# Performance work log

Measured on AMD Instinct MI355X. Metric: run time of the kernel, lower is better.

The kernel has to match this reference:

```python
import jax, jax.numpy as jnp
import numpy as np
import math

LOG_2PI = math.log(2.0 * math.pi)


def setup_inputs() -> dict:
    key = jax.random.key(0)
    k_x, k_mu = jax.random.split(key, 2)
    B, T, S, M, D = 8, 4096, 64, 8, 128
    return {
        "X": jax.random.normal(k_x, (B, T, D), dtype=jnp.float32),
        "pi_logits": jnp.zeros((S,), dtype=jnp.float32),
        "trans_logits": jnp.zeros((S, S), dtype=jnp.float32),
        "weight_logits": jnp.zeros((S, M), dtype=jnp.float32),
        "means": jax.random.normal(k_mu, (S, M, D), dtype=jnp.float32),
        "log_vars": jnp.zeros((S, M, D), dtype=jnp.float32),
    }


def reference(X, pi_logits, trans_logits, weight_logits, means, log_vars):
    # X: [B,T,D]; means/log_vars: [S,M,D]
    D = X.shape[-1]
    inv_vars = jnp.exp(-log_vars)                                   # [S,M,D]
    # -0.5 * sum_d (x_d - mu_d)^2 / var_d, expanded as GEMMs (same math):
    a = jnp.einsum('btd,smd->btsm', X * X, inv_vars)                # sum x^2/var
    b = jnp.einsum('btd,smd->btsm', X, means * inv_vars)            # sum x*mu/var
    c = jnp.sum(means * means * inv_vars, axis=-1)                  # [S,M]
    exp_term = -0.5 * (a - 2.0 * b + c[None, None, :, :])           # [B,T,S,M]
    log_norm = -0.5 * (jnp.sum(log_vars, axis=-1) + D * LOG_2PI)    # [S,M]
    log_mix_w = jax.nn.log_softmax(weight_logits, axis=1)           # [S,M]
    # emission log-prob per state: logsumexp over mixture components
    emis = jax.scipy.special.logsumexp(
        exp_term + (log_norm + log_mix_w)[None, None], axis=-1)     # [B,T,S]

    log_pi = jax.nn.log_softmax(pi_logits)                          # [S]
    log_A = jax.nn.log_softmax(trans_logits, axis=1)                # [S,S]

    alpha0 = log_pi[None, :] + emis[:, 0]                           # [B,S]
    emis_t = jnp.swapaxes(emis, 0, 1)                               # [T,B,S]

    def step(alpha, e_t):
        # alpha: [B,S]; log-semiring matvec: logsumexp_i(alpha_i + A_ij)
        nxt = e_t + jax.scipy.special.logsumexp(
            alpha[:, :, None] + log_A[None, :, :], axis=1)
        return nxt, None

    alpha_T, _ = jax.lax.scan(step, alpha0, emis_t[1:])
    return jax.scipy.special.logsumexp(alpha_T, axis=-1)            # [B]
```

## Files before the change

kernel.cpp:

```cpp
#include <hip/hip_runtime.h>
#include <hip/hip_bf16.h>
#include <math.h>

#define LOG2PI_F 1.8378770664093453f

typedef __attribute__((ext_vector_type(8))) short bf16x8;
typedef __attribute__((ext_vector_type(4))) float f32x4;
typedef __attribute__((ext_vector_type(16))) float f32x16;

static __device__ inline short f2bf(float x) {
  __hip_bfloat16 h = __float2bfloat16(x);
  return *reinterpret_cast<short*>(&h);
}
static __device__ inline unsigned cvtpk(float lo, float hi) {
  unsigned r;
  asm("v_cvt_pk_bf16_f32 %0, %1, %2" : "=v"(r) : "v"(lo), "v"(hi));
  return r;
}
static __device__ inline f32x4 mfma16(bf16x8 a, bf16x8 b, f32x4 c) {
  return __builtin_amdgcn_mfma_f32_16x16x32_bf16(a, b, c, 0, 0, 0);
}
static __device__ inline f32x16 mfma32(bf16x8 a, bf16x8 b, f32x16 c) {
  return __builtin_amdgcn_mfma_f32_32x32x16_bf16(a, b, c, 0, 0, 0);
}

__global__ __launch_bounds__(256) void mmm_prep_fused(
    const float* __restrict__ tl, const float* __restrict__ means,
    const float* __restrict__ log_vars, const float* __restrict__ weight_logits,
    const float* __restrict__ X,
    short* __restrict__ WTbf, short* __restrict__ Gt,
    float* __restrict__ const_c, short* __restrict__ XeP) {
  __shared__ float red[4];
  int bid = blockIdx.x;
  int tid = threadIdx.x;

  if (bid < 64) {
    if (tid < 64) {
      int r = bid, lane = tid;
      float v = tl[r * 64 + lane];
      float mx = v;
      #pragma unroll
      for (int off = 1; off < 64; off <<= 1) mx = fmaxf(mx, __shfl_xor(mx, off));
      float e = expf(v - mx);
      float s = e;
      #pragma unroll
      for (int off = 1; off < 64; off <<= 1) s += __shfl_xor(s, off);
      WTbf[lane * 64 + r] = f2bf(e / s);
    }
    return;
  }

  if (bid < 320) {
    int h = tid >> 7, d = tid & 127;
    int sm = (bid - 64) * 2 + h;
    int s = sm >> 3, m = sm & 7;
    float lv = log_vars[sm * 128 + d];
    float iv = expf(-lv);
    float mu = means[sm * 128 + d];
    float miv = mu * iv;
    Gt[sm * 256 + d] = f2bf(miv);
    Gt[sm * 256 + 128 + d] = f2bf(-0.5f * iv);
    float v = mu * miv + lv;
    #pragma unroll
    for (int off = 1; off < 64; off <<= 1) v += __shfl_xor(v, off);
    if ((tid & 63) == 0) red[tid >> 6] = v;
    __syncthreads();
    if (d == 0) {
      float tot = red[2 * h] + red[2 * h + 1];
      float wl[8];
      float mx = -3.4e38f;
      #pragma unroll
      for (int j = 0; j < 8; ++j) { wl[j] = weight_logits[s * 8 + j]; mx = fmaxf(mx, wl[j]); }
      float sum = 0.f;
      #pragma unroll
      for (int j = 0; j < 8; ++j) sum += expf(wl[j] - mx);
      float lmw = wl[m] - mx - logf(sum);
      const_c[sm] = -0.5f * (tot + 128.0f * LOG2PI_F) + lmw;
    }
    return;
  }

  int kbid = bid - 320;
  int q = kbid >> 7;
  int bt = ((kbid & 127) << 8) + tid;
  const float4* src = (const float4*)(X + (size_t)bt * 128 + q * 32);
  float xv[32];
  #pragma unroll
  for (int i = 0; i < 8; ++i) {
    float4 v = src[i];
    xv[4 * i] = v.x; xv[4 * i + 1] = v.y; xv[4 * i + 2] = v.z; xv[4 * i + 3] = v.w;
  }
  size_t base1 = ((size_t)q * 32768 + bt) * 32;
  size_t base2 = ((size_t)(q + 4) * 32768 + bt) * 32;
  int bx = bt & 3;
  #pragma unroll
  for (int g = 0; g < 4; ++g) {
    unsigned w1[4], w2[4];
    #pragma unroll
    for (int j = 0; j < 4; ++j) {
      float a = xv[g * 8 + 2 * j], c = xv[g * 8 + 2 * j + 1];
      w1[j] = cvtpk(a, c);
      w2[j] = cvtpk(a * a, c * c);
    }
    int gs = (g ^ bx) * 8;
    *(uint4*)&XeP[base1 + gs] = *(uint4*)w1;
    *(uint4*)&XeP[base2 + gs] = *(uint4*)w2;
  }
}

__global__ __launch_bounds__(512) void mmm_emis_kernel(
    const short* __restrict__ Gt, const short* __restrict__ XeP,
    const float* __restrict__ const_c,
    float* __restrict__ ehat, float* __restrict__ cmax) {
  __shared__ __align__(16) short Bt[16384];
  __shared__ __align__(16) float ccs[512];
  __shared__ float wavemax[8][64];
  __shared__ float colmax[64];
  int tid = threadIdx.x;
  int w = tid >> 6, lane = tid & 63, lr = lane & 15, lg = lane >> 4;

  ccs[tid] = const_c[tid];

  bf16x8 gf[4][8];
  #pragma unroll
  for (int rt = 0; rt < 4; ++rt) {
    int row = w * 64 + rt * 16 + lr;
    #pragma unroll
    for (int kc = 0; kc < 8; ++kc)
      gf[rt][kc] = *(const bf16x8*)&Gt[row * 256 + kc * 32 + lg * 8];
  }

  uint4 sreg[4];
  {
    size_t bt0 = (size_t)blockIdx.x * 64;
    #pragma unroll
    for (int r = 0; r < 4; ++r) {
      int ofs = r * 8192 + tid * 16;
      int kb2 = ofs >> 12, rem = ofs & 4095;
      sreg[r] = *(const uint4*)((const char*)XeP + ((size_t)kb2 * 32768 + bt0) * 64 + rem);
    }
  }

  for (int it = 0; it < 2; ++it) {
    int bt0 = (blockIdx.x + it * 256) * 64;
    __syncthreads();
    #pragma unroll
    for (int r = 0; r < 4; ++r)
      *(uint4*)((char*)Bt + r * 8192 + tid * 16) = sreg[r];
    __syncthreads();
    if (it == 0) {
      size_t bt0n = ((size_t)blockIdx.x + 256) * 64;
      #pragma unroll
      for (int r = 0; r < 4; ++r) {
        int ofs = r * 8192 + tid * 16;
        int kb2 = ofs >> 12, rem = ofs & 4095;
        sreg[r] = *(const uint4*)((const char*)XeP + ((size_t)kb2 * 32768 + bt0n) * 64 + rem);
      }
    }

    f32x4 acc[4][4];
    #pragma unroll
    for (int rt = 0; rt < 4; ++rt)
      #pragma unroll
      for (int ct = 0; ct < 4; ++ct)
        acc[rt][ct] = (f32x4){0.f, 0.f, 0.f, 0.f};

    #pragma unroll
    for (int kc = 0; kc < 8; ++kc) {
      bf16x8 bfr[4];
      #pragma unroll
      for (int ct = 0; ct < 4; ++ct) {
        int btL = ct * 16 + lr;
        bfr[ct] = *(const bf16x8*)&Bt[kc * 2048 + btL * 32 + ((lg ^ (btL & 3)) * 8)];
      }
      #pragma unroll
      for (int rt = 0; rt < 4; ++rt)
        #pragma unroll
        for (int ct = 0; ct < 4; ++ct)
          acc[rt][ct] = mfma16(gf[rt][kc], bfr[ct], acc[rt][ct]);
    }

    float lse[4][4];
    #pragma unroll
    for (int rt = 0; rt < 4; ++rt) {
      f32x4 cc = *(f32x4*)&ccs[w * 64 + rt * 16 + lg * 4];
      #pragma unroll
      for (int ct = 0; ct < 4; ++ct) {
        f32x4 v = acc[rt][ct] + cc;
        float mx = fmaxf(fmaxf(v[0], v[1]), fmaxf(v[2], v[3]));
        mx = fmaxf(mx, __shfl_xor(mx, 16));
        float sum = expf(v[0] - mx) + expf(v[1] - mx) + expf(v[2] - mx) + expf(v[3] - mx);
        sum += __shfl_xor(sum, 16);
        lse[rt][ct] = mx + logf(sum);
      }
    }
    #pragma unroll
    for (int ct = 0; ct < 4; ++ct) {
      float cm = fmaxf(fmaxf(lse[0][ct], lse[1][ct]), fmaxf(lse[2][ct], lse[3][ct]));
      cm = fmaxf(cm, __shfl_xor(cm, 32));
      if (lg == 0) wavemax[w][ct * 16 + lr] = cm;
    }
    __syncthreads();
    if (w == 0) {
      float cm = wavemax[0][lane];
      #pragma unroll
      for (int ww = 1; ww < 8; ++ww) cm = fmaxf(cm, wavemax[ww][lane]);
      colmax[lane] = cm;
      cmax[(size_t)bt0 + lane] = cm;
    }
    __syncthreads();
    #pragma unroll
    for (int ct = 0; ct < 4; ++ct) {
      float cm = colmax[ct * 16 + lr];
      #pragma unroll
      for (int rt = 0; rt < 4; ++rt) {
        float v = expf(lse[rt][ct] - cm);
        if (!(lg & 1))
          ehat[((size_t)bt0 + ct * 16 + lr) * 64 + (w * 8 + rt * 2 + (lg >> 1))] = v;
      }
    }
  }
}

__global__ __launch_bounds__(64) void mmm_chunk_kernel(
    const short* __restrict__ WTbf, const float* __restrict__ ehat,
    const float* __restrict__ cmax, short* __restrict__ NTb,
    float* __restrict__ aux) {
  __shared__ __align__(16) float elds[1024];
  int chunk = blockIdx.x, b = blockIdx.y;
  int lane = threadIdx.x;
  int l31 = lane & 31, hi = lane >> 5;

  int t0 = (chunk == 0) ? 1 : chunk * 16;
  int nsteps = (chunk == 0) ? 15 : 16;
  const float* eb = ehat + (size_t)b * 4096 * 64;

  {
    const float* esrc = eb + (size_t)t0 * 64;
    #pragma unroll
    for (int r = 0; r < 4; ++r)
      *(f32x4*)&elds[r * 256 + lane * 4] = *(const f32x4*)&esrc[r * 256 + lane * 4];
  }

  bf16x8 af[2][4];
  #pragma unroll
  for (int wi = 0; wi < 2; ++wi)
    #pragma unroll
    for (int kb = 0; kb < 4; ++kb)
      af[wi][kb] = *(const bf16x8*)&WTbf[(wi * 32 + l31) * 64 + kb * 16 + hi * 8];

  unsigned P[2][2][4][2];
  #pragma unroll
  for (int s = 0; s < 2; ++s) {
    int col = s * 32 + l31;
    #pragma unroll
    for (int cm = 0; cm < 2; ++cm)
      #pragma unroll
      for (int q = 0; q < 4; ++q)
        #pragma unroll
        for (int p = 0; p < 2; ++p) {
          int row = 32 * cm + 8 * q + 4 * hi + 2 * p;
          unsigned lo = (row == col) ? 0x3F80u : 0u;
          unsigned h16 = (row + 1 == col) ? 0x3F80u : 0u;
          P[s][cm][q][p] = lo | (h16 << 16);
        }
  }

  __syncthreads();

  float logscale = 0.f;
  f32x4 ecur[2][4], enxt[2][4];
  #pragma unroll
  for (int cm = 0; cm < 2; ++cm)
    #pragma unroll
    for (int q = 0; q < 4; ++q)
      ecur[cm][q] = *(const f32x4*)&elds[cm * 32 + q * 8 + hi * 4];

  for (int it = 0; it < nsteps; ++it) {
    if (it + 1 < nsteps) {
      #pragma unroll
      for (int cm = 0; cm < 2; ++cm)
        #pragma unroll
        for (int q = 0; q < 4; ++q)
          enxt[cm][q] = *(const f32x4*)&elds[(it + 1) * 64 + cm * 32 + q * 8 + hi * 4];
    }

    __builtin_amdgcn_s_setprio(1);
    #pragma unroll
    for (int s = 0; s < 2; ++s) {
      bf16x8 B[4];
      #pragma unroll
      for (int kb = 0; kb < 4; ++kb) {
        int cm = kb >> 1, kbl = kb & 1;
        int4 wrd;
        #pragma unroll
        for (int p = 0; p < 2; ++p) {
          unsigned avv = P[s][cm][2 * kbl + 1][p];
          unsigned bvv = P[s][cm][2 * kbl][p];
          asm("v_permlane32_swap_b32 %0, %1" : "+v"(avv), "+v"(bvv));
          if (p == 0) { wrd.x = (int)bvv; wrd.z = (int)avv; }
          else        { wrd.y = (int)bvv; wrd.w = (int)avv; }
        }
        B[kb] = *(bf16x8*)&wrd;
      }

      f32x16 d0, d1;
      #pragma unroll
      for (int r = 0; r < 16; ++r) { d0[r] = 0.f; d1[r] = 0.f; }
      #pragma unroll
      for (int kb = 0; kb < 4; ++kb) {
        d0 = mfma32(af[0][kb], B[kb], d0);
        d1 = mfma32(af[1][kb], B[kb], d1);
      }

      #pragma unroll
      for (int q = 0; q < 4; ++q)
        #pragma unroll
        for (int p = 0; p < 2; ++p) {
          P[s][0][q][p] = cvtpk(d0[4 * q + 2 * p] * ecur[0][q][2 * p],
                                d0[4 * q + 2 * p + 1] * ecur[0][q][2 * p + 1]);
          P[s][1][q][p] = cvtpk(d1[4 * q + 2 * p] * ecur[1][q][2 * p],
                                d1[4 * q + 2 * p + 1] * ecur[1][q][2 * p + 1]);
        }
    }
    __builtin_amdgcn_s_setprio(0);

    if ((it & 7) == 7) {
      float m = 0.f;
      #pragma unroll
      for (int s = 0; s < 2; ++s)
        #pragma unroll
        for (int cm = 0; cm < 2; ++cm)
          #pragma unroll
          for (int q = 0; q < 4; ++q)
            #pragma unroll
            for (int p = 0; p < 2; ++p) {
              unsigned u = P[s][cm][q][p];
              m = fmaxf(m, __uint_as_float(u << 16));
              m = fmaxf(m, __uint_as_float(u & 0xffff0000u));
            }
      #pragma unroll
      for (int off = 1; off < 64; off <<= 1) m = fmaxf(m, __shfl_xor(m, off));
      float inv = 1.0f / m;
      #pragma unroll
      for (int s = 0; s < 2; ++s)
        #pragma unroll
        for (int cm = 0; cm < 2; ++cm)
          #pragma unroll
          for (int q = 0; q < 4; ++q)
            #pragma unroll
            for (int p = 0; p < 2; ++p) {
              unsigned u = P[s][cm][q][p];
              P[s][cm][q][p] = cvtpk(__uint_as_float(u << 16) * inv,
                                     __uint_as_float(u & 0xffff0000u) * inv);
            }
      logscale += logf(m);
    }

    #pragma unroll
    for (int cm = 0; cm < 2; ++cm)
      #pragma unroll
      for (int q = 0; q < 4; ++q) ecur[cm][q] = enxt[cm][q];
  }

  unsigned short* No = (unsigned short*)(NTb + (((size_t)b * 256 + chunk) << 12));
  #pragma unroll
  for (int s = 0; s < 2; ++s)
    #pragma unroll
    for (int cm = 0; cm < 2; ++cm)
      #pragma unroll
      for (int q = 0; q < 4; ++q)
        #pragma unroll
        for (int p = 0; p < 2; ++p) {
          int row = 32 * cm + 8 * q + 4 * hi + 2 * p;
          int col = s * 32 + l31;
          unsigned u = P[s][cm][q][p];
          No[row * 64 + col] = (unsigned short)(u & 0xffffu);
          No[(row + 1) * 64 + col] = (unsigned short)(u >> 16);
        }

  float cs = (lane < nsteps) ? cmax[(size_t)b * 4096 + t0 + lane] : 0.f;
  #pragma unroll
  for (int off = 1; off < 64; off <<= 1) cs += __shfl_xor(cs, off);
  if (lane == 0) aux[(size_t)b * 256 + chunk] = cs + logscale;
}

__global__ __launch_bounds__(256) void mmm_merge_kernel(
    const short* __restrict__ NTb, const float* __restrict__ aux,
    float* __restrict__ G2T, float* __restrict__ auxg) {
  int g = blockIdx.x, b = blockIdx.y;
  int tid = threadIdx.x;
  int w = tid >> 6, lane = tid & 63;
  int wi = w >> 1, wj = w & 1;
  int lr = lane & 15, lg = lane >> 4;

  __shared__ __align__(16) short L[2][4096];
  __shared__ float wmax[4];

  for (int idx = tid; idx < 4096; idx += 256) {
    int j = idx >> 6, k = idx & 63;
    L[0][idx ^ ((j & 7) << 3)] = (j == k) ? (short)0x3F80 : (short)0;
  }
  __syncthreads();

  int cbase = b * 256 + g * 8;

  float logscale = 0.f;
  int cur = 0;
  f32x4 acc[2][2];

  bf16x8 apre[2][2];
  {
    const short* Mc = NTb + ((size_t)cbase << 12);
    #pragma unroll
    for (int rt = 0; rt < 2; ++rt)
      #pragma unroll
      for (int kc = 0; kc < 2; ++kc)
        apre[rt][kc] = *(const bf16x8*)&Mc[(wi * 32 + rt * 16 + lr) * 64 + kc * 32 + lg * 8];
  }

  for (int cc = 0; cc < 8; ++cc) {
    bf16x8 acur[2][2];
    #pragma unroll
    for (int rt = 0; rt < 2; ++rt)
      #pragma unroll
      for (int kc = 0; kc < 2; ++kc) acur[rt][kc] = apre[rt][kc];
    if (cc < 7) {
      const short* Mc = NTb + ((size_t)(cbase + cc + 1) << 12);
      #pragma unroll
      for (int rt = 0; rt < 2; ++rt)
        #pragma unroll
        for (int kc = 0; kc < 2; ++kc)
          apre[rt][kc] = *(const bf16x8*)&Mc[(wi * 32 + rt * 16 + lr) * 64 + kc * 32 + lg * 8];
    }

    logscale += aux[cbase + cc];

    bf16x8 bfr[2][2];
    #pragma unroll
    for (int ct = 0; ct < 2; ++ct) {
      int j = wj * 32 + ct * 16 + lr;
      int sw = (j & 7) << 3;
      #pragma unroll
      for (int kc = 0; kc < 2; ++kc)
        bfr[ct][kc] = *(const bf16x8*)&L[cur][(j * 64 + kc * 32 + lg * 8) ^ sw];
    }

    #pragma unroll
    for (int rt = 0; rt < 2; ++rt)
      #pragma unroll
      for (int ct = 0; ct < 2; ++ct) {
        f32x4 c = {0.f, 0.f, 0.f, 0.f};
        c = mfma16(acur[rt][0], bfr[ct][0], c);
        c = mfma16(acur[rt][1], bfr[ct][1], c);
        acc[rt][ct] = c;
      }

    if ((cc & 3) == 3) {
      float m = 0.f;
      #pragma unroll
      for (int rt = 0; rt < 2; ++rt)
        #pragma unroll
        for (int ct = 0; ct < 2; ++ct)
          #pragma unroll
          for (int r = 0; r < 4; ++r) m = fmaxf(m, acc[rt][ct][r]);
      #pragma unroll
      for (int off = 1; off < 64; off <<= 1) m = fmaxf(m, __shfl_xor(m, off));
      if (lane == 0) wmax[w] = m;
      __syncthreads();
      m = fmaxf(fmaxf(wmax[0], wmax[1]), fmaxf(wmax[2], wmax[3]));
      float inv = 1.0f / m;
      #pragma unroll
      for (int rt = 0; rt < 2; ++rt)
        #pragma unroll
        for (int ct = 0; ct < 2; ++ct) acc[rt][ct] *= inv;
      logscale += logf(m);
    }

    int nxt = cur ^ 1;
    unsigned* L32 = (unsigned*)&L[nxt][0];
    #pragma unroll
    for (int rt = 0; rt < 2; ++rt)
      #pragma unroll
      for (int ct = 0; ct < 2; ++ct) {
        int row0 = wi * 32 + rt * 16 + lg * 4;
        int col = wj * 32 + ct * 16 + lr;
        int sidx = (col * 64 + row0) ^ ((col & 7) << 3);
        L32[(sidx >> 1) + 0] = cvtpk(acc[rt][ct][0], acc[rt][ct][1]);
        L32[(sidx >> 1) + 1] = cvtpk(acc[rt][ct][2], acc[rt][ct][3]);
      }
    __syncthreads();
    cur = nxt;
  }

  float* Mo = G2T + (((size_t)b * 32 + g) << 12);
  #pragma unroll
  for (int rt = 0; rt < 2; ++rt)
    #pragma unroll
    for (int ct = 0; ct < 2; ++ct)
      #pragma unroll
      for (int r = 0; r < 4; ++r) {
        int row = wi * 32 + rt * 16 + lg * 4 + r;
        int col = wj * 32 + ct * 16 + lr;
        Mo[row * 64 + col] = acc[rt][ct][r];
      }

  if (w == 0 && lane == 0) auxg[b * 32 + g] = logscale;
}

__global__ __launch_bounds__(64) void mmm_combine_kernel(
    const float* __restrict__ pi_logits, const float* __restrict__ ehat,
    const float* __restrict__ cmax, const float* __restrict__ G2T,
    const float* __restrict__ auxg, float* __restrict__ out) {
  int b = blockIdx.x, lane = threadIdx.x;
  __shared__ __align__(16) float alds[64];

  float pv = pi_logits[lane];
  float mx = pv;
  #pragma unroll
  for (int off = 1; off < 64; off <<= 1) mx = fmaxf(mx, __shfl_xor(mx, off));
  float pe = expf(pv - mx);
  float ps = pe;
  #pragma unroll
  for (int off = 1; off < 64; off <<= 1) ps += __shfl_xor(ps, off);

  float a = (pe / ps) * ehat[(size_t)b * 4096 * 64 + lane];
  double logtot = (double)cmax[(size_t)b * 4096];
  alds[lane] = a;
  __builtin_amdgcn_wave_barrier();

  const float* Mb = G2T + (((size_t)b * 32) << 12) + lane * 64;
  f32x4 mc[16], mn[16];
  #pragma unroll
  for (int i = 0; i < 16; ++i) mc[i] = *(const f32x4*)&Mb[i * 4];

  for (int g = 0; g < 32; ++g) {
    if (g < 31) {
      const float* Mn = Mb + ((size_t)(g + 1) << 12);
      #pragma unroll
      for (int i = 0; i < 16; ++i) mn[i] = *(const f32x4*)&Mn[i * 4];
    }
    f32x4 a4 = {0.f, 0.f, 0.f, 0.f};
    #pragma unroll
    for (int i = 0; i < 16; ++i) {
      f32x4 av = *(const f32x4*)&alds[i * 4];
      a4 += mc[i] * av;
    }
    float acc = (a4[0] + a4[1]) + (a4[2] + a4[3]);
    float s = acc;
    #pragma unroll
    for (int off = 1; off < 64; off <<= 1) s += __shfl_xor(s, off);
    logtot += (double)(auxg[b * 32 + g] + logf(s));
    float an = acc / s;
    __builtin_amdgcn_wave_barrier();
    alds[lane] = an;
    __builtin_amdgcn_wave_barrier();
    #pragma unroll
    for (int i = 0; i < 16; ++i) mc[i] = mn[i];
  }
  if (lane == 0) out[b] = (float)logtot;
}

extern "C" void kernel_launch(void* const* d_in, const int* in_sizes, int n_in,
                              void* d_out, int out_size, void* d_ws, size_t ws_size,
                              hipStream_t stream) {
  const float* X      = (const float*)d_in[0];
  const float* pi_l   = (const float*)d_in[1];
  const float* tr_l   = (const float*)d_in[2];
  const float* wl     = (const float*)d_in[3];
  const float* means  = (const float*)d_in[4];
  const float* lvs    = (const float*)d_in[5];
  float* out = (float*)d_out;

  float* ws = (float*)d_ws;
  short* Gt      = (short*)ws;
  float* const_c = ws + 65536;
  short* WTbf    = (short*)(ws + 66048);
  float* cmaxp   = ws + 68608;
  float* ehat    = ws + 101376;
  short* XeP     = (short*)(ws + 2198528);
  short* NTb     = (short*)(ws + 2198528);
  float* aux     = ws + 6392832;
  float* G2T     = ws + 6396928;
  float* auxg    = ws + 7445504;

  mmm_prep_fused<<<832, 256, 0, stream>>>(tr_l, means, lvs, wl, X,
                                          WTbf, Gt, const_c, XeP);
  mmm_emis_kernel<<<256, 512, 0, stream>>>(Gt, XeP, const_c, ehat, cmaxp);
  mmm_chunk_kernel<<<dim3(256, 8), 64, 0, stream>>>(WTbf, ehat, cmaxp, NTb, aux);
  mmm_merge_kernel<<<dim3(32, 8), 256, 0, stream>>>(NTb, aux, G2T, auxg);
  mmm_combine_kernel<<<8, 64, 0, stream>>>(pi_l, ehat, cmaxp, G2T, auxg, out);
}
```

Baseline: 113.7 us.

## Fuse emission and chunk-product kernels through shared memory

Merges the emission kernel and the per-chunk transition-product kernel into one launch. Scaled emissions and column maxima now stay in LDS and feed the 16-step chunk recurrences directly, with 8 waves each handling one chunk. The full ehat/cmax round trip through global memory and one launch are removed, and only the t=0 values are kept for the combine step. In exchange the chunk work now runs on 256 blocks of 512 threads instead of 2048 single-wave blocks, which lowers parallelism, and LDS use per block grows by 32KB, which may cut occupancy.

```diff
diff --git a/kernel.cpp b/kernel.cpp
--- a/kernel.cpp
+++ b/kernel.cpp
@@ -108,16 +108,19 @@
   }
 }
 
-__global__ __launch_bounds__(512) void mmm_emis_kernel(
+__global__ __launch_bounds__(512) void mmm_emischunk_kernel(
     const short* __restrict__ Gt, const short* __restrict__ XeP,
-    const float* __restrict__ const_c,
-    float* __restrict__ ehat, float* __restrict__ cmax) {
+    const float* __restrict__ const_c, const short* __restrict__ WTbf,
+    short* __restrict__ NTb, float* __restrict__ aux,
+    float* __restrict__ ehat0, float* __restrict__ cmax0) {
   __shared__ __align__(16) short Bt[16384];
   __shared__ __align__(16) float ccs[512];
   __shared__ float wavemax[8][64];
-  __shared__ float colmax[64];
+  __shared__ float colmax2[2][64];
+  __shared__ __align__(16) float elds[2][4096];
   int tid = threadIdx.x;
   int w = tid >> 6, lane = tid & 63, lr = lane & 15, lg = lane >> 4;
+  int T0 = (blockIdx.x & 63) * 64;
 
   ccs[tid] = const_c[tid];
 
@@ -142,7 +145,7 @@
   }
 
   for (int it = 0; it < 2; ++it) {
-    int bt0 = (blockIdx.x + it * 256) * 64;
+    int bcur = (blockIdx.x + it * 256) >> 6;
     __syncthreads();
     #pragma unroll
     for (int r = 0; r < 4; ++r)
@@ -205,42 +208,33 @@
       float cm = wavemax[0][lane];
       #pragma unroll
       for (int ww = 1; ww < 8; ++ww) cm = fmaxf(cm, wavemax[ww][lane]);
-      colmax[lane] = cm;
-      cmax[(size_t)bt0 + lane] = cm;
+      colmax2[it][lane] = cm;
+      if (lane == 0 && T0 == 0) cmax0[bcur] = cm;
     }
     __syncthreads();
     #pragma unroll
     for (int ct = 0; ct < 4; ++ct) {
-      float cm = colmax[ct * 16 + lr];
+      float cm = colmax2[it][ct * 16 + lr];
       #pragma unroll
       for (int rt = 0; rt < 4; ++rt) {
         float v = expf(lse[rt][ct] - cm);
-        if (!(lg & 1))
-          ehat[((size_t)bt0 + ct * 16 + lr) * 64 + (w * 8 + rt * 2 + (lg >> 1))] = v;
-      }
-    }
-  }
-}
-
-__global__ __launch_bounds__(64) void mmm_chunk_kernel(
-    const short* __restrict__ WTbf, const float* __restrict__ ehat,
-    const float* __restrict__ cmax, short* __restrict__ NTb,
-    float* __restrict__ aux) {
-  __shared__ __align__(16) float elds[1024];
-  int chunk = blockIdx.x, b = blockIdx.y;
-  int lane = threadIdx.x;
+        if (!(lg & 1)) {
+          int s = w * 8 + rt * 2 + (lg >> 1);
+          elds[it][(ct * 16 + lr) * 64 + s] = v;
+          if (T0 == 0 && ct == 0 && lr == 0) ehat0[bcur * 64 + s] = v;
+        }
+      }
+    }
+  }
+  __syncthreads();
+
+  int tl = w >> 2, q = w & 3;
+  int bS = (blockIdx.x + tl * 256) >> 6;
+  int c = (T0 >> 4) + q;
+  int t0l, nsteps;
+  if (c == 0) { t0l = 1; nsteps = 15; } else { t0l = q * 16; nsteps = 16; }
   int l31 = lane & 31, hi = lane >> 5;
-
-  int t0 = (chunk == 0) ? 1 : chunk * 16;
-  int nsteps = (chunk == 0) ? 15 : 16;
-  const float* eb = ehat + (size_t)b * 4096 * 64;
-
-  {
-    const float* esrc = eb + (size_t)t0 * 64;
-    #pragma unroll
-    for (int r = 0; r < 4; ++r)
-      *(f32x4*)&elds[r * 256 + lane * 4] = *(const f32x4*)&esrc[r * 256 + lane * 4];
-  }
+  const float* etile = &elds[tl][0];
 
   bf16x8 af[2][4];
   #pragma unroll
@@ -256,33 +250,31 @@
     #pragma unroll
     for (int cm = 0; cm < 2; ++cm)
       #pragma unroll
-      for (int q = 0; q < 4; ++q)
+      for (int qq = 0; qq < 4; ++qq)
         #pragma unroll
         for (int p = 0; p < 2; ++p) {
-          int row = 32 * cm + 8 * q + 4 * hi + 2 * p;
+          int row = 32 * cm + 8 * qq + 4 * hi + 2 * p;
           unsigned lo = (row == col) ? 0x3F80u : 0u;
           unsigned h16 = (row + 1 == col) ? 0x3F80u : 0u;
-          P[s][cm][q][p] = lo | (h16 << 16);
+          P[s][cm][qq][p] = lo | (h16 << 16);
         }
   }
-
-  __syncthreads();
 
   float logscale = 0.f;
   f32x4 ecur[2][4], enxt[2][4];
   #pragma unroll
   for (int cm = 0; cm < 2; ++cm)
     #pragma unroll
-    for (int q = 0; q < 4; ++q)
-      ecur[cm][q] = *(const f32x4*)&elds[cm * 32 + q * 8 + hi * 4];
-
-  for (int it = 0; it < nsteps; ++it) {
-    if (it + 1 < nsteps) {
+    for (int qq = 0; qq < 4; ++qq)
+      ecur[cm][qq] = *(const f32x4*)&etile[t0l * 64 + cm * 32 + qq * 8 + hi * 4];
+
+  for (int i = 0; i < nsteps; ++i) {
+    if (i + 1 < nsteps) {
       #pragma unroll
       for (int cm = 0; cm < 2; ++cm)
         #pragma unroll
-        for (int q = 0; q < 4; ++q)
-          enxt[cm][q] = *(const f32x4*)&elds[(it + 1) * 64 + cm * 32 + q * 8 + hi * 4];
+        for (int qq = 0; qq < 4; ++qq)
+          enxt[cm][qq] = *(const f32x4*)&etile[(t0l + i + 1) * 64 + cm * 32 + qq * 8 + hi * 4];
     }
 
     __builtin_amdgcn_s_setprio(1);
@@ -314,28 +306,28 @@
       }
 
       #pragma unroll
-      for (int q = 0; q < 4; ++q)
+      for (int qq = 0; qq < 4; ++qq)
         #pragma unroll
         for (int p = 0; p < 2; ++p) {
-          P[s][0][q][p] = cvtpk(d0[4 * q + 2 * p] * ecur[0][q][2 * p],
-                                d0[4 * q + 2 * p + 1] * ecur[0][q][2 * p + 1]);
-          P[s][1][q][p] = cvtpk(d1[4 * q + 2 * p] * ecur[1][q][2 * p],
-                                d1[4 * q + 2 * p + 1] * ecur[1][q][2 * p + 1]);
+          P[s][0][qq][p] = cvtpk(d0[4 * qq + 2 * p] * ecur[0][qq][2 * p],
+                                 d0[4 * qq + 2 * p + 1] * ecur[0][qq][2 * p + 1]);
+          P[s][1][qq][p] = cvtpk(d1[4 * qq + 2 * p] * ecur[1][qq][2 * p],
+                                 d1[4 * qq + 2 * p + 1] * ecur[1][qq][2 * p + 1]);
         }
     }
     __builtin_amdgcn_s_setprio(0);
 
-    if ((it & 7) == 7) {
+    if ((i & 7) == 7) {
       float m = 0.f;
       #pragma unroll
       for (int s = 0; s < 2; ++s)
         #pragma unroll
         for (int cm = 0; cm < 2; ++cm)
           #pragma unroll
-          for (int q = 0; q < 4; ++q)
+          for (int qq = 0; qq < 4; ++qq)
             #pragma unroll
             for (int p = 0; p < 2; ++p) {
-              unsigned u = P[s][cm][q][p];
+              unsigned u = P[s][cm][qq][p];
               m = fmaxf(m, __uint_as_float(u << 16));
               m = fmaxf(m, __uint_as_float(u & 0xffff0000u));
             }
@@ -347,12 +339,12 @@
         #pragma unroll
         for (int cm = 0; cm < 2; ++cm)
           #pragma unroll
-          for (int q = 0; q < 4; ++q)
+          for (int qq = 0; qq < 4; ++qq)
             #pragma unroll
             for (int p = 0; p < 2; ++p) {
-              unsigned u = P[s][cm][q][p];
-              P[s][cm][q][p] = cvtpk(__uint_as_float(u << 16) * inv,
-                                     __uint_as_float(u & 0xffff0000u) * inv);
+              unsigned u = P[s][cm][qq][p];
+              P[s][cm][qq][p] = cvtpk(__uint_as_float(u << 16) * inv,
+                                      __uint_as_float(u & 0xffff0000u) * inv);
             }
       logscale += logf(m);
     }
@@ -360,29 +352,29 @@
     #pragma unroll
     for (int cm = 0; cm < 2; ++cm)
       #pragma unroll
-      for (int q = 0; q < 4; ++q) ecur[cm][q] = enxt[cm][q];
-  }
-
-  unsigned short* No = (unsigned short*)(NTb + (((size_t)b * 256 + chunk) << 12));
+      for (int qq = 0; qq < 4; ++qq) ecur[cm][qq] = enxt[cm][qq];
+  }
+
+  unsigned short* No = (unsigned short*)(NTb + (((size_t)bS * 256 + c) << 12));
   #pragma unroll
   for (int s = 0; s < 2; ++s)
     #pragma unroll
     for (int cm = 0; cm < 2; ++cm)
       #pragma unroll
-      for (int q = 0; q < 4; ++q)
+      for (int qq = 0; qq < 4; ++qq)
         #pragma unroll
         for (int p = 0; p < 2; ++p) {
-          int row = 32 * cm + 8 * q + 4 * hi + 2 * p;
+          int row = 32 * cm + 8 * qq + 4 * hi + 2 * p;
           int col = s * 32 + l31;
-          unsigned u = P[s][cm][q][p];
+          unsigned u = P[s][cm][qq][p];
           No[row * 64 + col] = (unsigned short)(u & 0xffffu);
           No[(row + 1) * 64 + col] = (unsigned short)(u >> 16);
         }
 
-  float cs = (lane < nsteps) ? cmax[(size_t)b * 4096 + t0 + lane] : 0.f;
+  float cs = (lane < nsteps) ? colmax2[tl][t0l + lane] : 0.f;
   #pragma unroll
   for (int off = 1; off < 64; off <<= 1) cs += __shfl_xor(cs, off);
-  if (lane == 0) aux[(size_t)b * 256 + chunk] = cs + logscale;
+  if (lane == 0) aux[(size_t)bS * 256 + c] = cs + logscale;
 }
 
 __global__ __launch_bounds__(256) void mmm_merge_kernel(
@@ -509,8 +501,8 @@
 }
 
 __global__ __launch_bounds__(64) void mmm_combine_kernel(
-    const float* __restrict__ pi_logits, const float* __restrict__ ehat,
-    const float* __restrict__ cmax, const float* __restrict__ G2T,
+    const float* __restrict__ pi_logits, const float* __restrict__ ehat0,
+    const float* __restrict__ cmax0, const float* __restrict__ G2T,
     const float* __restrict__ auxg, float* __restrict__ out) {
   int b = blockIdx.x, lane = threadIdx.x;
   __shared__ __align__(16) float alds[64];
@@ -524,8 +516,8 @@
   #pragma unroll
   for (int off = 1; off < 64; off <<= 1) ps += __shfl_xor(ps, off);
 
-  float a = (pe / ps) * ehat[(size_t)b * 4096 * 64 + lane];
-  double logtot = (double)cmax[(size_t)b * 4096];
+  float a = (pe / ps) * ehat0[b * 64 + lane];
+  double logtot = (double)cmax0[b];
   alds[lane] = a;
   __builtin_amdgcn_wave_barrier();
 
@@ -576,18 +568,18 @@
   short* Gt      = (short*)ws;
   float* const_c = ws + 65536;
   short* WTbf    = (short*)(ws + 66048);
-  float* cmaxp   = ws + 68608;
-  float* ehat    = ws + 101376;
+  float* ehat0   = ws + 68096;
+  float* cmax0   = ws + 68608;
   short* XeP     = (short*)(ws + 2198528);
-  short* NTb     = (short*)(ws + 2198528);
-  float* aux     = ws + 6392832;
-  float* G2T     = ws + 6396928;
-  float* auxg    = ws + 7445504;
+  short* NTb     = (short*)(ws + 6392832);
+  float* aux     = ws + 10587136;
+  float* G2T     = ws + 10591232;
+  float* auxg    = ws + 11639808;
 
   mmm_prep_fused<<<832, 256, 0, stream>>>(tr_l, means, lvs, wl, X,
                                           WTbf, Gt, const_c, XeP);
-  mmm_emis_kernel<<<256, 512, 0, stream>>>(Gt, XeP, const_c, ehat, cmaxp);
-  mmm_chunk_kernel<<<dim3(256, 8), 64, 0, stream>>>(WTbf, ehat, cmaxp, NTb, aux);
+  mmm_emischunk_kernel<<<256, 512, 0, stream>>>(Gt, XeP, const_c, WTbf,
+                                                NTb, aux, ehat0, cmax0);
   mmm_merge_kernel<<<dim3(32, 8), 256, 0, stream>>>(NTb, aux, G2T, auxg);
-  mmm_combine_kernel<<<8, 64, 0, stream>>>(pi_l, ehat, cmaxp, G2T, auxg, out);
-}
+  mmm_combine_kernel<<<8, 64, 0, stream>>>(pi_l, ehat0, cmax0, G2T, auxg, out);
+}
```

New measurement: 101.8 us. 10.5% less time.
